# Kernel optimization log

Hardware: AMD Instinct MI355X
Metric: run time of the kernel (lower is better)

The kernel has to match this reference:

```python
import jax, jax.numpy as jnp
import numpy as np

H = 4          # num_heads
K_HOP = 2
EPS = 1e-5


def _ln(x, g, b):
    m = jnp.mean(x, axis=-1, keepdims=True)
    v = jnp.mean((x - m) ** 2, axis=-1, keepdims=True)
    return (x - m) * jax.lax.rsqrt(v + EPS) * g + b


def setup_inputs() -> dict:
    key = jax.random.key(0)
    B, T, N, D = 16, 24, 512, 64
    F = 256
    ks = jax.random.split(key, 16)
    s = 0.02
    inp = {
        'x': jax.random.normal(ks[0], (B, T, N, D), dtype=jnp.float32),
        'adj': jax.random.uniform(ks[1], (N, N), dtype=jnp.float32),
        'Wq': jax.random.normal(ks[2], (D, D), dtype=jnp.float32) * s,
        'bq': jnp.zeros((D,), jnp.float32),
        'Wk': jax.random.normal(ks[3], (D, D), dtype=jnp.float32) * s,
        'bk': jnp.zeros((D,), jnp.float32),
        'Wv': jax.random.normal(ks[4], (D, D), dtype=jnp.float32) * s,
        'bv': jnp.zeros((D,), jnp.float32),
        'Wo': jax.random.normal(ks[5], (D, D), dtype=jnp.float32) * s,
        'bo': jnp.zeros((D,), jnp.float32),
        'gcW': jax.random.normal(ks[6], (K_HOP + 1, D, D), dtype=jnp.float32) * s,
        'gcb': jnp.zeros((K_HOP + 1, D), jnp.float32),
        'W1': jax.random.normal(ks[7], (D, F), dtype=jnp.float32) * s,
        'b1': jnp.zeros((F,), jnp.float32),
        'W2': jax.random.normal(ks[8], (F, D), dtype=jnp.float32) * s,
        'b2': jnp.zeros((D,), jnp.float32),
        'g_t': jnp.ones((D,), jnp.float32), 'b_t': jnp.zeros((D,), jnp.float32),
        'g_g': jnp.ones((D,), jnp.float32), 'b_g': jnp.zeros((D,), jnp.float32),
        'g_f': jnp.ones((D,), jnp.float32), 'b_f': jnp.zeros((D,), jnp.float32),
    }
    return inp


def _forward(x, adj, Wq, bq, Wk, bk, Wv, bv, Wo, bo, gcW, gcb,
             W1, b1, W2, b2, g_t, b_t, g_g, b_g, g_f, b_f):
    B, T, N, D = x.shape
    hd = D // H
    scale = hd ** -0.5

    # ---- temporal multi-head attention (per node, along T) ----
    def heads(y):
        return y.reshape(B, T, N, H, hd)
    q = heads(x @ Wq + bq)
    k = heads(x @ Wk + bk)
    v = heads(x @ Wv + bv)
    scores = jnp.einsum('bqnhd,bknhd->bnhqk', q, k) * scale  # [B,N,H,T,T]
    attn = jax.nn.softmax(scores, axis=-1)
    att = jnp.einsum('bnhqk,bknhd->bqnhd', attn, v).reshape(B, T, N, D)
    att = att @ Wo + bo
    h = _ln(x + att, g_t, b_t)

    # ---- K-hop graph convolution: sum_k A_hat^k X W_k ----
    A = adj + jnp.eye(N, dtype=adj.dtype)
    deg = A.sum(-1)
    dinv = jnp.clip(deg, 1e-12, None) ** -0.5
    Ahat = dinv[:, None] * A * dinv[None, :]  # [N,N], shared across B*T
    prop = h
    gout = prop @ gcW[0] + gcb[0]
    for kk in range(1, K_HOP + 1):
        prop = jnp.einsum('mn,btnd->btmd', Ahat, prop)
        gout = gout + prop @ gcW[kk] + gcb[kk]
    h = _ln(h + gout, g_g, b_g)

    # ---- FFN (exact GELU, as torch default) ----
    f = jax.nn.gelu(h @ W1 + b1, approximate=False) @ W2 + b2
    return _ln(h + f, g_f, b_f)


def reference(x, adj, Wq, bq, Wk, bk, Wv, bv, Wo, bo, gcW, gcb,
              W1, b1, W2, b2, g_t, b_t, g_g, b_g, g_f, b_f):
    return _forward(x, adj, Wq, bq, Wk, bk, Wv, bv, Wo, bo, gcW, gcb,
                    W1, b1, W2, b2, g_t, b_t, g_g, b_g, g_f, b_f)
```

## Files before the change

### kernel.cpp

```cpp
#include <hip/hip_runtime.h>
#include <hip/hip_bf16.h>
#include <math.h>

typedef __hip_bfloat16 bf16;
typedef unsigned short ushort_t;

__device__ __forceinline__ float us2f(ushort_t u){
  union { unsigned u; float f; } v; v.u = ((unsigned)u) << 16; return v.f;
}
__device__ __forceinline__ ushort_t f2us(float f){
  union { float f; unsigned u; } v; v.f = f;
  unsigned r = v.u + 0x7fff + ((v.u >> 16) & 1);
  return (ushort_t)(r >> 16);
}

__device__ __forceinline__ float gelu_f(float x){
  float y = x * fmaf(0.0356774081f, x*x, 0.7978845608f);
  float e = __expf(-2.0f*y);
  return x * __builtin_amdgcn_rcpf(1.0f + e);
}

#define B_ 16
#define T_ 24
#define N_ 512
#define D_ 64
#define F_ 256

typedef __attribute__((ext_vector_type(8)))  short  frag8;
typedef __attribute__((ext_vector_type(16))) float  accv16;

__device__ __forceinline__ float wave_sum(float v){
#pragma unroll
  for (int off = 32; off > 0; off >>= 1) v += __shfl_xor(v, off, 64);
  return v;
}

__global__ __launch_bounds__(64) void k_dinv(const float* __restrict__ adj,
                                             float* __restrict__ dinv){
  int m = blockIdx.x;
  float s = 0.f;
  for (int n = threadIdx.x; n < N_; n += 64) s += adj[m*N_ + n];
  s = wave_sum(s);
  if (threadIdx.x == 0){
    float deg = s + 1.0f;
    dinv[m] = rsqrtf(fmaxf(deg, 1e-12f));
  }
}

__global__ __launch_bounds__(256) void k_ahat(const float* __restrict__ adj,
                                              const float* __restrict__ dinv,
                                              ushort_t* __restrict__ AhatB){
  int idx = blockIdx.x*256 + threadIdx.x;
  int m = idx >> 9, n = idx & (N_-1);
  float a = adj[idx] + (m == n ? 1.f : 0.f);
  AhatB[idx] = f2us(dinv[m]*a*dinv[n]);
}

__global__ __launch_bounds__(256) void k_wprep(
    const float* __restrict__ W1, const float* __restrict__ W2,
    const float* __restrict__ Wq, const float* __restrict__ Wk,
    const float* __restrict__ Wv, const float* __restrict__ Wo,
    const float* __restrict__ gcW,
    ushort_t* __restrict__ W1t, ushort_t* __restrict__ W2t,
    ushort_t* __restrict__ Wqt, ushort_t* __restrict__ Wkt,
    ushort_t* __restrict__ Wvt, ushort_t* __restrict__ Wot,
    ushort_t* __restrict__ gWt){
  int o = blockIdx.x*256 + threadIdx.x;
  int f = o >> 6, e = o & 63;
  W1t[o] = f2us(W1[e*256 + f]);
  int d = o >> 8, e2 = o & 255;
  W2t[o] = f2us(W2[e2*64 + d]);
  if (o < 4096){
    int dd = o >> 6, ee = o & 63;
    Wqt[o] = f2us(Wq[ee*64 + dd]);
    Wkt[o] = f2us(Wk[ee*64 + dd]);
    Wvt[o] = f2us(Wv[ee*64 + dd]);
    Wot[o] = f2us(Wo[ee*64 + dd]);
    gWt[o]        = f2us(gcW[       ee*64 + dd]);
    gWt[4096 + o] = f2us(gcW[4096 + ee*64 + dd]);
    gWt[8192 + o] = f2us(gcW[8192 + ee*64 + dd]);
  }
}

__global__ __launch_bounds__(256, 4) void k_attn_m(
    const float* __restrict__ x,
    const ushort_t* __restrict__ Wqt, const float* __restrict__ bq,
    const ushort_t* __restrict__ Wkt, const float* __restrict__ bk,
    const ushort_t* __restrict__ Wvt, const float* __restrict__ bv,
    const ushort_t* __restrict__ Wot, const float* __restrict__ bo,
    const float* __restrict__ g_t, const float* __restrict__ b_t,
    float* __restrict__ h1)
{
  __shared__ __align__(16) char smem[37120];
  ushort_t (*xsA)[72] = (ushort_t(*)[72]) smem;
  ushort_t (*qs)[72]  = (ushort_t(*)[72])(smem + 6912);
  ushort_t (*ks)[72]  = (ushort_t(*)[72])(smem + 13824);
  float    (*Os)[65]  = (float(*)[65])   (smem + 6912);
  ushort_t *vsT       = (ushort_t*)(smem + 20736);

  int tid = threadIdx.x;
  int lane = tid & 63, w = tid >> 6;
  int l31 = lane & 31, lh = lane >> 5;
  int mt = (w >> 1) * 32, nt = (w & 1) * 32;
  int b = blockIdx.x >> 8;
  int n0 = (blockIdx.x & 255) * 2;

  {
    uint4 z4 = {0,0,0,0};
#pragma unroll
    for (int i = 0; i < 4; i++)
      *(uint4*)(smem + 20736 + (tid + i*256)*16) = z4;
  }
#pragma unroll
  for (int i = 0; i < 3; i++){
    int idx = tid + i*256;
    int row = idx >> 4, d4 = (idx & 15) * 4;
    int node = row >= 24;
    int t = row - node*24;
    const float4 v = *(const float4*)&x[(((size_t)b*T_ + t)*N_ + n0 + node)*D_ + d4];
    ushort_t tmp[4] = { f2us(v.x), f2us(v.y), f2us(v.z), f2us(v.w) };
    *(unsigned long long*)&xsA[row][d4] = *(unsigned long long*)tmp;
  }
  __syncthreads();

#pragma unroll
  for (int pj = 0; pj < 3; pj++){
    const ushort_t* Wp = (pj==0 ? Wqt : pj==1 ? Wkt : Wvt);
    accv16 a = {};
#pragma unroll
    for (int kk = 0; kk < 64; kk += 16){
      frag8 af = *(const frag8*)&xsA[mt + l31][kk + lh*8];
      frag8 bf = *(const frag8*)&Wp[(size_t)(nt + l31)*64 + kk + lh*8];
      a = __builtin_amdgcn_mfma_f32_32x32x16_bf16(af, bf, a, 0, 0, 0);
    }
    float bias = (pj==0 ? bq : pj==1 ? bk : bv)[nt + l31];
    if (pj < 2){
      ushort_t (*dst)[72] = (pj==0 ? qs : ks);
#pragma unroll
      for (int r = 0; r < 16; r++){
        int row = mt + (r & 3) + 8*(r >> 2) + 4*lh;
        if (row < 48) dst[row][nt + l31] = f2us(a[r] + bias);
      }
    } else {
      int cl = nt + l31;
      int vr0 = ((cl >> 4) << 5) + (cl & 15);
#pragma unroll
      for (int r = 0; r < 16; r++){
        int row = mt + (r & 3) + 8*(r >> 2) + 4*lh;
        if (row < 48){
          int node = (row >= 24);
          int t2 = row - node*24;
          int R = node*128 + vr0;
          vsT[R*32 + (((t2 >> 3) ^ ((R >> 1) & 3)) << 3) + (t2 & 7)] = f2us(a[r] + bias);
        }
      }
    }
  }
  __syncthreads();

  int vs_s = (l31 >> 1) & 3;
#pragma unroll
  for (int gi = 0; gi < 2; gi++){
    int g = w*2 + gi;
    int node = g >> 2, hh = g & 3;
    accv16 s = {};
    frag8 kf = *(const frag8*)&ks[node*24 + l31][hh*16 + lh*8];
    frag8 qf = *(const frag8*)&qs[node*24 + l31][hh*16 + lh*8];
    s = __builtin_amdgcn_mfma_f32_32x32x16_bf16(kf, qf, s, 0, 0, 0);
    float e[12]; float sm = 0.f;
#pragma unroll
    for (int r = 0; r < 12; r++){ e[r] = __expf(s[r]*0.25f); sm += e[r]; }
    sm += __shfl_xor(sm, 32, 64);
    float rinv = 1.0f / sm;
    union { unsigned long long q; ushort_t u[4]; } a0, a1, a2;
#pragma unroll
    for (int j = 0; j < 4; j++){
      a0.u[j] = f2us(e[j]   * rinv);
      a1.u[j] = f2us(e[4+j] * rinv);
      a2.u[j] = f2us(e[8+j] * rinv);
    }
    unsigned long long send1 = lh ? a0.q : a1.q;
    unsigned long long r1 = __shfl_xor(send1, 32, 64);
    unsigned long long r2 = __shfl_xor(a2.q, 32, 64);
    union { frag8 f; unsigned long long q[2]; } f0, f1;
    f0.q[0] = lh ? r1   : a0.q;
    f0.q[1] = lh ? a1.q : r1;
    f1.q[0] = lh ? 0ULL : a2.q;
    f1.q[1] = lh ? 0ULL : r2;
    const ushort_t* vb = &vsT[(g*32 + l31)*32];
    frag8 bf0 = *(const frag8*)&vb[((0 + lh) ^ vs_s) << 3];
    frag8 bf1 = *(const frag8*)&vb[((2 + lh) ^ vs_s) << 3];
    accv16 acc = {};
    acc = __builtin_amdgcn_mfma_f32_32x32x16_bf16(f0.f, bf0, acc, 0, 0, 0);
    acc = __builtin_amdgcn_mfma_f32_32x32x16_bf16(f1.f, bf1, acc, 0, 0, 0);
    if (l31 < 16){
#pragma unroll
      for (int r = 0; r < 12; r++){
        int row = (r & 3) + 8*(r >> 2) + 4*lh;
        xsA[node*24 + row][hh*16 + l31] = f2us(acc[r]);
      }
    }
  }
  __syncthreads();

  accv16 ao = {};
#pragma unroll
  for (int kk = 0; kk < 64; kk += 16){
    frag8 af = *(const frag8*)&xsA[mt + l31][kk + lh*8];
    frag8 bf = *(const frag8*)&Wot[(size_t)(nt + l31)*64 + kk + lh*8];
    ao = __builtin_amdgcn_mfma_f32_32x32x16_bf16(af, bf, ao, 0, 0, 0);
  }
  {
    float bov = bo[nt + l31];
#pragma unroll
    for (int r = 0; r < 16; r++){
      int row = mt + (r & 3) + 8*(r >> 2) + 4*lh;
      if (row < 48) Os[row][nt + l31] = ao[r] + bov;
    }
  }
  __syncthreads();
  {
    float gv = g_t[lane], bvv = b_t[lane];
#pragma unroll
    for (int i = 0; i < 12; i++){
      int row = w + i*4;
      int node = row >= 24;
      int t = row - node*24;
      size_t gaddr = (((size_t)b*T_ + t)*N_ + n0 + node)*D_ + lane;
      float v = Os[row][lane] + x[gaddr];
      float m = wave_sum(v) * (1.f/64.f);
      float df = v - m;
      float var = wave_sum(df*df) * (1.f/64.f);
      h1[gaddr] = df * rsqrtf(var + 1e-5f) * gv + bvv;
    }
  }
}

__global__ __launch_bounds__(256, 8) void k_hT(const float* __restrict__ h,
                                               ushort_t* __restrict__ hT){
  __shared__ __align__(16) ushort_t tb[64][76];
  int tid = threadIdx.x;
  int n0 = (blockIdx.x & 7) * 64;
  size_t bt = blockIdx.x >> 3;
  const float* src = h + (bt*N_ + n0)*D_;
#pragma unroll
  for (int i = 0; i < 4; i++){
    int q = tid + i*256;
    int row = q >> 4, d4 = (q & 15)*4;
    float4 v = *(const float4*)&src[(size_t)q*4];
    ushort_t tmp[4] = { f2us(v.x), f2us(v.y), f2us(v.z), f2us(v.w) };
    *(unsigned long long*)&tb[row][d4] = *(unsigned long long*)tmp;
  }
  __syncthreads();
  int d = tid >> 2, nseg = (tid & 3)*16;
  ushort_t tmp[16];
#pragma unroll
  for (int j = 0; j < 16; j++){
    int jj = (j + ((d & 7) << 1)) & 15;
    tmp[jj] = tb[nseg + jj][d];
  }
  ushort_t* dst = hT + (bt*D_ + d)*N_ + n0 + nseg;
  *(uint4*)&dst[0] = *(uint4*)&tmp[0];
  *(uint4*)&dst[8] = *(uint4*)&tmp[8];
}

__global__ __launch_bounds__(256, 5) void k_prop_m(
    const ushort_t* __restrict__ Ahat,
    const ushort_t* __restrict__ XT,
    const ushort_t* __restrict__ gWkt,
    ushort_t* __restrict__ PT,
    ushort_t* __restrict__ G,
    int store_p, int accum)
{
  __shared__ __align__(16) ushort_t Ab[64][72];
  __shared__ __align__(16) ushort_t Xb[64][72];
  __shared__ __align__(16) ushort_t Yt[64][72];
  int tid  = threadIdx.x;
  int lane = tid & 63, w = tid >> 6;
  int mw = (w >> 1) * 32, nw = (w & 1) * 32;
  int l31 = lane & 31, lh = lane >> 5;
  int m0 = blockIdx.x * 64;
  size_t slice = (size_t)blockIdx.y * (N_ * D_);
  const ushort_t* Xg = XT + slice;

  accv16 acc = {};
  int ar = tid >> 3, ac8 = (tid & 7) * 8;
  for (int k0 = 0; k0 < N_; k0 += 64){
#pragma unroll
    for (int g = 0; g < 2; g++){
      int rr = ar + g*32;
      *(uint4*)&Ab[rr][ac8] = *(const uint4*)&Ahat[(size_t)(m0 + rr)*N_ + k0 + ac8];
      *(uint4*)&Xb[rr][ac8] = *(const uint4*)&Xg[(size_t)rr*N_ + k0 + ac8];
    }
    __syncthreads();
#pragma unroll
    for (int kk = 0; kk < 64; kk += 16){
      frag8 af = *(const frag8*)&Ab[mw + l31][kk + lh*8];
      frag8 bf = *(const frag8*)&Xb[nw + l31][kk + lh*8];
      acc = __builtin_amdgcn_mfma_f32_32x32x16_bf16(af, bf, acc, 0, 0, 0);
    }
    __syncthreads();
  }

#pragma unroll
  for (int r = 0; r < 16; r++){
    int row = mw + (r & 3) + 8*(r >> 2) + 4*lh;
    Yt[row][nw + l31] = f2us(acc[r]);
  }
  __syncthreads();

  if (store_p){
    int d = tid >> 2, mseg = (tid & 3) * 16;
    ushort_t tmp[16];
#pragma unroll
    for (int j = 0; j < 16; j++){
      int jj = (j + ((d & 7) << 1)) & 15;
      tmp[jj] = Yt[mseg + jj][d];
    }
    ushort_t* dst = PT + slice + (size_t)d*N_ + m0 + mseg;
    *(uint4*)&dst[0] = *(uint4*)&tmp[0];
    *(uint4*)&dst[8] = *(uint4*)&tmp[8];
  }

  accv16 acc2 = {};
#pragma unroll
  for (int kk = 0; kk < 64; kk += 16){
    frag8 af = *(const frag8*)&Yt[mw + l31][kk + lh*8];
    frag8 bf = *(const frag8*)&gWkt[(size_t)(nw + l31)*64 + kk + lh*8];
    acc2 = __builtin_amdgcn_mfma_f32_32x32x16_bf16(af, bf, acc2, 0, 0, 0);
  }
#pragma unroll
  for (int r = 0; r < 16; r++){
    int row = mw + (r & 3) + 8*(r >> 2) + 4*lh;
    Ab[row][nw + l31] = f2us(acc2[r]);
  }
  __syncthreads();
#pragma unroll
  for (int g = 0; g < 2; g++){
    int rr = ar + g*32;
    uint4 vv = *(const uint4*)&Ab[rr][ac8];
    size_t base = slice + (size_t)(m0 + rr)*D_ + ac8;
    if (accum){
      uint4 ov = *(const uint4*)&G[base];
      ushort_t* s = (ushort_t*)&vv;
      ushort_t* o = (ushort_t*)&ov;
      ushort_t res[8];
#pragma unroll
      for (int i = 0; i < 8; i++) res[i] = f2us(us2f(s[i]) + us2f(o[i]));
      *(uint4*)&G[base] = *(uint4*)res;
    } else {
      *(uint4*)&G[base] = vv;
    }
  }
}

__global__ __launch_bounds__(256, 4) void k_cffn(
  const ushort_t* __restrict__ g12,
  const ushort_t* __restrict__ gW0t,
  const float* __restrict__ gcb,
  const float* __restrict__ g_g, const float* __restrict__ b_g,
  const ushort_t* __restrict__ W1t, const ushort_t* __restrict__ W2t,
  const float* __restrict__ b1, const float* __restrict__ b2,
  const float* __restrict__ g_f, const float* __restrict__ b_f,
  float* __restrict__ h)
{
  __shared__ __align__(16) char smem[26624];
  ushort_t (*hsA)[72] = (ushort_t(*)[72]) smem;
  ushort_t (*Uc)[136] = (ushort_t(*)[136])(smem + 9216);
  float    (*Sf)[68]  = (float(*)[68])    (smem + 9216);
  float    (*Os)[68]  = (float(*)[68])    (smem + 9216);

  int tid = threadIdx.x;
  int lane = tid & 63, w = tid >> 6;
  int l31 = lane & 31, lh = lane >> 5;
  size_t tok0 = (size_t)blockIdx.x * 64;

#pragma unroll
  for (int i = 0; i < 4; i++){
    int q = tid + i*256;
    int row = q >> 4, d4 = (q & 15) * 4;
    float4 v = *(const float4*)&h[tok0*64 + (size_t)q*4];
    ushort_t tmp[4] = { f2us(v.x), f2us(v.y), f2us(v.z), f2us(v.w) };
    *(unsigned long long*)&hsA[row][d4] = *(unsigned long long*)tmp;
  }
  __syncthreads();

  {
    int mg = (w >> 1) * 32, ng = (w & 1) * 32;
    accv16 ag = {};
#pragma unroll
    for (int kk = 0; kk < 64; kk += 16){
      frag8 af = *(const frag8*)&hsA[mg + l31][kk + lh*8];
      frag8 bf = *(const frag8*)&gW0t[(size_t)(ng + l31)*64 + kk + lh*8];
      ag = __builtin_amdgcn_mfma_f32_32x32x16_bf16(af, bf, ag, 0, 0, 0);
    }
    int col = ng + l31;
    float bs = gcb[col] + gcb[64 + col] + gcb[128 + col];
#pragma unroll
    for (int r = 0; r < 16; r++){
      int row = mg + (r & 3) + 8*(r >> 2) + 4*lh;
      size_t ga = (tok0 + row)*64 + col;
      Sf[row][col] = ag[r] + h[ga] + us2f(g12[ga]) + bs;
    }
  }
  __syncthreads();

  int rrow = tid >> 2, seg = (tid & 3) * 16;
  float h2r[16];
  {
    float vb[16]; float s1 = 0.f;
#pragma unroll
    for (int j4 = 0; j4 < 4; j4++){
      float4 v = *(const float4*)&Sf[rrow][seg + j4*4];
      vb[j4*4+0] = v.x; vb[j4*4+1] = v.y; vb[j4*4+2] = v.z; vb[j4*4+3] = v.w;
      s1 += v.x + v.y + v.z + v.w;
    }
    s1 += __shfl_xor(s1, 1, 64); s1 += __shfl_xor(s1, 2, 64);
    float m = s1 * (1.f/64.f);
    float s2 = 0.f;
#pragma unroll
    for (int j = 0; j < 16; j++){ vb[j] -= m; s2 += vb[j]*vb[j]; }
    s2 += __shfl_xor(s2, 1, 64); s2 += __shfl_xor(s2, 2, 64);
    float rstd = rsqrtf(s2 * (1.f/64.f) + 1e-5f);
    ushort_t tmp[16];
#pragma unroll
    for (int j4 = 0; j4 < 4; j4++){
      float4 gv = *(const float4*)&g_g[seg + j4*4];
      float4 bv = *(const float4*)&b_g[seg + j4*4];
      h2r[j4*4+0] = vb[j4*4+0]*rstd*gv.x + bv.x;
      h2r[j4*4+1] = vb[j4*4+1]*rstd*gv.y + bv.y;
      h2r[j4*4+2] = vb[j4*4+2]*rstd*gv.z + bv.z;
      h2r[j4*4+3] = vb[j4*4+3]*rstd*gv.w + bv.w;
    }
#pragma unroll
    for (int j = 0; j < 16; j++) tmp[j] = f2us(h2r[j]);
    *(uint4*)&hsA[rrow][seg]     = *(uint4*)&tmp[0];
    *(uint4*)&hsA[rrow][seg + 8] = *(uint4*)&tmp[8];
  }
  __syncthreads();

  int mw1 = (w & 1) * 32, nA = (w >> 1) * 32;
  int mw2 = (w >> 1) * 32, dw = (w & 1) * 32;
  accv16 acc2 = {};
#pragma unroll
  for (int f0 = 0; f0 < F_; f0 += 128){
    if (f0) __syncthreads();
    accv16 accA = {}, accB = {};
#pragma unroll
    for (int kk = 0; kk < 64; kk += 16){
      frag8 af  = *(const frag8*)&hsA[mw1 + l31][kk + lh*8];
      frag8 b0  = *(const frag8*)&W1t[(size_t)(f0 + nA + l31)*64 + kk + lh*8];
      frag8 b1f = *(const frag8*)&W1t[(size_t)(f0 + nA + 64 + l31)*64 + kk + lh*8];
      accA = __builtin_amdgcn_mfma_f32_32x32x16_bf16(af, b0,  accA, 0, 0, 0);
      accB = __builtin_amdgcn_mfma_f32_32x32x16_bf16(af, b1f, accB, 0, 0, 0);
    }
    {
      float bA = b1[f0 + nA + l31];
      float bB = b1[f0 + nA + 64 + l31];
#pragma unroll
      for (int r = 0; r < 16; r++){
        int row = mw1 + (r & 3) + 8*(r >> 2) + 4*lh;
        Uc[row][nA + l31]      = f2us(gelu_f(accA[r] + bA));
        Uc[row][nA + 64 + l31] = f2us(gelu_f(accB[r] + bB));
      }
    }
    __syncthreads();
#pragma unroll
    for (int kk = 0; kk < 128; kk += 16){
      frag8 af = *(const frag8*)&Uc[mw2 + l31][kk + lh*8];
      frag8 bf = *(const frag8*)&W2t[(size_t)(dw + l31)*256 + f0 + kk + lh*8];
      acc2 = __builtin_amdgcn_mfma_f32_32x32x16_bf16(af, bf, acc2, 0, 0, 0);
    }
  }
  __syncthreads();
  {
    float b2v = b2[dw + l31];
#pragma unroll
    for (int r = 0; r < 16; r++){
      int row = mw2 + (r & 3) + 8*(r >> 2) + 4*lh;
      Os[row][dw + l31] = acc2[r] + b2v;
    }
  }
  __syncthreads();

  {
    float vb[16]; float s1 = 0.f;
#pragma unroll
    for (int j4 = 0; j4 < 4; j4++){
      float4 v = *(const float4*)&Os[rrow][seg + j4*4];
      vb[j4*4+0] = v.x + h2r[j4*4+0];
      vb[j4*4+1] = v.y + h2r[j4*4+1];
      vb[j4*4+2] = v.z + h2r[j4*4+2];
      vb[j4*4+3] = v.w + h2r[j4*4+3];
      s1 += vb[j4*4+0] + vb[j4*4+1] + vb[j4*4+2] + vb[j4*4+3];
    }
    s1 += __shfl_xor(s1, 1, 64); s1 += __shfl_xor(s1, 2, 64);
    float m = s1 * (1.f/64.f);
    float s2 = 0.f;
#pragma unroll
    for (int j = 0; j < 16; j++){ vb[j] -= m; s2 += vb[j]*vb[j]; }
    s2 += __shfl_xor(s2, 1, 64); s2 += __shfl_xor(s2, 2, 64);
    float rstd = rsqrtf(s2 * (1.f/64.f) + 1e-5f);
#pragma unroll
    for (int j4 = 0; j4 < 4; j4++){
      float4 gv = *(const float4*)&g_f[seg + j4*4];
      float4 bv = *(const float4*)&b_f[seg + j4*4];
      float4 st;
      st.x = vb[j4*4+0]*rstd*gv.x + bv.x;
      st.y = vb[j4*4+1]*rstd*gv.y + bv.y;
      st.z = vb[j4*4+2]*rstd*gv.z + bv.z;
      st.w = vb[j4*4+3]*rstd*gv.w + bv.w;
      *(float4*)&h[(tok0 + rrow)*64 + seg + j4*4] = st;
    }
  }
}

extern "C" void kernel_launch(void* const* d_in, const int* in_sizes, int n_in,
                              void* d_out, int out_size, void* d_ws, size_t ws_size,
                              hipStream_t stream)
{
  const float* x   = (const float*)d_in[0];
  const float* adj = (const float*)d_in[1];
  const float* Wq  = (const float*)d_in[2];
  const float* bq  = (const float*)d_in[3];
  const float* Wk  = (const float*)d_in[4];
  const float* bk  = (const float*)d_in[5];
  const float* Wv  = (const float*)d_in[6];
  const float* bv  = (const float*)d_in[7];
  const float* Wo  = (const float*)d_in[8];
  const float* bo  = (const float*)d_in[9];
  const float* gcW = (const float*)d_in[10];
  const float* gcb = (const float*)d_in[11];
  const float* W1  = (const float*)d_in[12];
  const float* b1  = (const float*)d_in[13];
  const float* W2  = (const float*)d_in[14];
  const float* b2  = (const float*)d_in[15];
  const float* g_t = (const float*)d_in[16];
  const float* b_t = (const float*)d_in[17];
  const float* g_g = (const float*)d_in[18];
  const float* b_g = (const float*)d_in[19];
  const float* g_f = (const float*)d_in[20];
  const float* b_f = (const float*)d_in[21];

  const size_t MD = (size_t)B_*T_*N_*D_;
  float* dinv = (float*)d_ws;
  ushort_t* AhatB = (ushort_t*)(dinv + 512);
  ushort_t* PT  = AhatB + (size_t)N_*N_;
  ushort_t* g12 = PT + MD;
  ushort_t* hT  = g12 + MD;
  ushort_t* W1t = hT + MD;
  ushort_t* W2t = W1t + 256*64;
  ushort_t* Wqt = W2t + 64*256;
  ushort_t* Wkt = Wqt + 4096;
  ushort_t* Wvt = Wkt + 4096;
  ushort_t* Wot = Wvt + 4096;
  ushort_t* gWt = Wot + 4096;
  float* h = (float*)d_out;

  k_dinv<<<N_, 64, 0, stream>>>(adj, dinv);
  k_ahat<<<(N_*N_)/256, 256, 0, stream>>>(adj, dinv, AhatB);
  k_wprep<<<64, 256, 0, stream>>>(W1, W2, Wq, Wk, Wv, Wo, gcW,
                                  W1t, W2t, Wqt, Wkt, Wvt, Wot, gWt);
  k_attn_m<<<B_*N_/2, 256, 0, stream>>>(x, Wqt,bq, Wkt,bk, Wvt,bv, Wot,bo, g_t,b_t, h);
  k_hT<<<B_*T_*8, 256, 0, stream>>>(h, hT);
  k_prop_m<<<dim3(N_/64, B_*T_), 256, 0, stream>>>(AhatB, hT, gWt + 4096, PT, g12, 1, 0);
  k_prop_m<<<dim3(N_/64, B_*T_), 256, 0, stream>>>(AhatB, PT, gWt + 8192, PT, g12, 0, 1);
  k_cffn<<<(int)(MD/D_/64), 256, 0, stream>>>(g12, gWt, gcb, g_g, b_g,
                                              W1t, W2t, b1, b2, g_f, b_f, h);
}
```

Measured before the change: 383.0 us.

## Precompute Ahat squared and fuse both graph-propagation hops into one kernel

A new kernel computes Ahat² once per call, reading Ahat and a transposed copy written by k_ahat. The two sequential propagation kernels become one k_gconv, which multiplies the hT tile by Ahat and by Ahat² in the same k-loop and applies both gcW projections before a single store. This removes the PT intermediate write and reread, the read-modify-write on G, and one launch, at the cost of an extra Ahat² tile load per step and a small N×N matmul. The bf16 conversion also switches to the compiler's native __bf16 cast, and rounding Ahat² to bf16 changes numerics slightly.

```diff
diff --git a/kernel.cpp b/kernel.cpp
--- a/kernel.cpp
+++ b/kernel.cpp
@@ -9,9 +9,7 @@
   union { unsigned u; float f; } v; v.u = ((unsigned)u) << 16; return v.f;
 }
 __device__ __forceinline__ ushort_t f2us(float f){
-  union { float f; unsigned u; } v; v.f = f;
-  unsigned r = v.u + 0x7fff + ((v.u >> 16) & 1);
-  return (ushort_t)(r >> 16);
+  union { __bf16 b; ushort_t u; } v; v.b = (__bf16)f; return v.u;
 }
 
 __device__ __forceinline__ float gelu_f(float x){
@@ -49,11 +47,59 @@
 
 __global__ __launch_bounds__(256) void k_ahat(const float* __restrict__ adj,
                                               const float* __restrict__ dinv,
-                                              ushort_t* __restrict__ AhatB){
+                                              ushort_t* __restrict__ AhatB,
+                                              ushort_t* __restrict__ AhatBT){
   int idx = blockIdx.x*256 + threadIdx.x;
   int m = idx >> 9, n = idx & (N_-1);
   float a = adj[idx] + (m == n ? 1.f : 0.f);
-  AhatB[idx] = f2us(dinv[m]*a*dinv[n]);
+  ushort_t v = f2us(dinv[m]*a*dinv[n]);
+  AhatB[idx] = v;
+  AhatBT[n*N_ + m] = v;
+}
+
+__global__ __launch_bounds__(256, 4) void k_ah2(
+    const ushort_t* __restrict__ A1,
+    const ushort_t* __restrict__ A1T,
+    ushort_t* __restrict__ A2)
+{
+  __shared__ __align__(16) ushort_t Ab[64][72];
+  __shared__ __align__(16) ushort_t Bb[64][72];
+  __shared__ __align__(16) ushort_t Yt[64][72];
+  int tid  = threadIdx.x;
+  int lane = tid & 63, w = tid >> 6;
+  int mw = (w >> 1) * 32, nw = (w & 1) * 32;
+  int l31 = lane & 31, lh = lane >> 5;
+  int m0 = blockIdx.x * 64, n0 = blockIdx.y * 64;
+  int ar = tid >> 3, ac8 = (tid & 7) * 8;
+
+  accv16 acc = {};
+  for (int k0 = 0; k0 < N_; k0 += 64){
+#pragma unroll
+    for (int g = 0; g < 2; g++){
+      int rr = ar + g*32;
+      *(uint4*)&Ab[rr][ac8] = *(const uint4*)&A1 [(size_t)(m0 + rr)*N_ + k0 + ac8];
+      *(uint4*)&Bb[rr][ac8] = *(const uint4*)&A1T[(size_t)(n0 + rr)*N_ + k0 + ac8];
+    }
+    __syncthreads();
+#pragma unroll
+    for (int kk = 0; kk < 64; kk += 16){
+      frag8 af = *(const frag8*)&Ab[mw + l31][kk + lh*8];
+      frag8 bf = *(const frag8*)&Bb[nw + l31][kk + lh*8];
+      acc = __builtin_amdgcn_mfma_f32_32x32x16_bf16(af, bf, acc, 0, 0, 0);
+    }
+    __syncthreads();
+  }
+#pragma unroll
+  for (int r = 0; r < 16; r++){
+    int row = mw + (r & 3) + 8*(r >> 2) + 4*lh;
+    Yt[row][nw + l31] = f2us(acc[r]);
+  }
+  __syncthreads();
+#pragma unroll
+  for (int g = 0; g < 2; g++){
+    int rr = ar + g*32;
+    *(uint4*)&A2[(size_t)(m0 + rr)*N_ + n0 + ac8] = *(const uint4*)&Yt[rr][ac8];
+  }
 }
 
 __global__ __launch_bounds__(256) void k_wprep(
@@ -264,15 +310,16 @@
   *(uint4*)&dst[8] = *(uint4*)&tmp[8];
 }
 
-__global__ __launch_bounds__(256, 5) void k_prop_m(
-    const ushort_t* __restrict__ Ahat,
+__global__ __launch_bounds__(256, 4) void k_gconv(
+    const ushort_t* __restrict__ A1,
+    const ushort_t* __restrict__ A2,
     const ushort_t* __restrict__ XT,
-    const ushort_t* __restrict__ gWkt,
-    ushort_t* __restrict__ PT,
-    ushort_t* __restrict__ G,
-    int store_p, int accum)
+    const ushort_t* __restrict__ gW1t,
+    const ushort_t* __restrict__ gW2t,
+    ushort_t* __restrict__ G)
 {
-  __shared__ __align__(16) ushort_t Ab[64][72];
+  __shared__ __align__(16) ushort_t Ab1[64][72];
+  __shared__ __align__(16) ushort_t Ab2[64][72];
   __shared__ __align__(16) ushort_t Xb[64][72];
   __shared__ __align__(16) ushort_t Yt[64][72];
   int tid  = threadIdx.x;
@@ -282,22 +329,25 @@
   int m0 = blockIdx.x * 64;
   size_t slice = (size_t)blockIdx.y * (N_ * D_);
   const ushort_t* Xg = XT + slice;
-
-  accv16 acc = {};
   int ar = tid >> 3, ac8 = (tid & 7) * 8;
+
+  accv16 acc1 = {}, acc2 = {};
   for (int k0 = 0; k0 < N_; k0 += 64){
 #pragma unroll
     for (int g = 0; g < 2; g++){
       int rr = ar + g*32;
-      *(uint4*)&Ab[rr][ac8] = *(const uint4*)&Ahat[(size_t)(m0 + rr)*N_ + k0 + ac8];
-      *(uint4*)&Xb[rr][ac8] = *(const uint4*)&Xg[(size_t)rr*N_ + k0 + ac8];
+      *(uint4*)&Ab1[rr][ac8] = *(const uint4*)&A1[(size_t)(m0 + rr)*N_ + k0 + ac8];
+      *(uint4*)&Ab2[rr][ac8] = *(const uint4*)&A2[(size_t)(m0 + rr)*N_ + k0 + ac8];
+      *(uint4*)&Xb [rr][ac8] = *(const uint4*)&Xg[(size_t)rr*N_ + k0 + ac8];
     }
     __syncthreads();
 #pragma unroll
     for (int kk = 0; kk < 64; kk += 16){
-      frag8 af = *(const frag8*)&Ab[mw + l31][kk + lh*8];
-      frag8 bf = *(const frag8*)&Xb[nw + l31][kk + lh*8];
-      acc = __builtin_amdgcn_mfma_f32_32x32x16_bf16(af, bf, acc, 0, 0, 0);
+      frag8 bf  = *(const frag8*)&Xb [nw + l31][kk + lh*8];
+      frag8 af1 = *(const frag8*)&Ab1[mw + l31][kk + lh*8];
+      frag8 af2 = *(const frag8*)&Ab2[mw + l31][kk + lh*8];
+      acc1 = __builtin_amdgcn_mfma_f32_32x32x16_bf16(af1, bf, acc1, 0, 0, 0);
+      acc2 = __builtin_amdgcn_mfma_f32_32x32x16_bf16(af2, bf, acc2, 0, 0, 0);
     }
     __syncthreads();
   }
@@ -305,52 +355,34 @@
 #pragma unroll
   for (int r = 0; r < 16; r++){
     int row = mw + (r & 3) + 8*(r >> 2) + 4*lh;
-    Yt[row][nw + l31] = f2us(acc[r]);
-  }
-  __syncthreads();
-
-  if (store_p){
-    int d = tid >> 2, mseg = (tid & 3) * 16;
-    ushort_t tmp[16];
-#pragma unroll
-    for (int j = 0; j < 16; j++){
-      int jj = (j + ((d & 7) << 1)) & 15;
-      tmp[jj] = Yt[mseg + jj][d];
-    }
-    ushort_t* dst = PT + slice + (size_t)d*N_ + m0 + mseg;
-    *(uint4*)&dst[0] = *(uint4*)&tmp[0];
-    *(uint4*)&dst[8] = *(uint4*)&tmp[8];
-  }
-
-  accv16 acc2 = {};
+    Yt [row][nw + l31] = f2us(acc1[r]);
+    Ab1[row][nw + l31] = f2us(acc2[r]);
+  }
+  __syncthreads();
+
+  accv16 ag = {};
 #pragma unroll
   for (int kk = 0; kk < 64; kk += 16){
-    frag8 af = *(const frag8*)&Yt[mw + l31][kk + lh*8];
-    frag8 bf = *(const frag8*)&gWkt[(size_t)(nw + l31)*64 + kk + lh*8];
-    acc2 = __builtin_amdgcn_mfma_f32_32x32x16_bf16(af, bf, acc2, 0, 0, 0);
+    frag8 a1f = *(const frag8*)&Yt [mw + l31][kk + lh*8];
+    frag8 b1f = *(const frag8*)&gW1t[(size_t)(nw + l31)*64 + kk + lh*8];
+    ag = __builtin_amdgcn_mfma_f32_32x32x16_bf16(a1f, b1f, ag, 0, 0, 0);
+  }
+#pragma unroll
+  for (int kk = 0; kk < 64; kk += 16){
+    frag8 a2f = *(const frag8*)&Ab1[mw + l31][kk + lh*8];
+    frag8 b2f = *(const frag8*)&gW2t[(size_t)(nw + l31)*64 + kk + lh*8];
+    ag = __builtin_amdgcn_mfma_f32_32x32x16_bf16(a2f, b2f, ag, 0, 0, 0);
   }
 #pragma unroll
   for (int r = 0; r < 16; r++){
     int row = mw + (r & 3) + 8*(r >> 2) + 4*lh;
-    Ab[row][nw + l31] = f2us(acc2[r]);
+    Xb[row][nw + l31] = f2us(ag[r]);
   }
   __syncthreads();
 #pragma unroll
   for (int g = 0; g < 2; g++){
     int rr = ar + g*32;
-    uint4 vv = *(const uint4*)&Ab[rr][ac8];
-    size_t base = slice + (size_t)(m0 + rr)*D_ + ac8;
-    if (accum){
-      uint4 ov = *(const uint4*)&G[base];
-      ushort_t* s = (ushort_t*)&vv;
-      ushort_t* o = (ushort_t*)&ov;
-      ushort_t res[8];
-#pragma unroll
-      for (int i = 0; i < 8; i++) res[i] = f2us(us2f(s[i]) + us2f(o[i]));
-      *(uint4*)&G[base] = *(uint4*)res;
-    } else {
-      *(uint4*)&G[base] = vv;
-    }
+    *(uint4*)&G[slice + (size_t)(m0 + rr)*D_ + ac8] = *(const uint4*)&Xb[rr][ac8];
   }
 }
 
@@ -543,10 +575,12 @@
   const float* b_f = (const float*)d_in[21];
 
   const size_t MD = (size_t)B_*T_*N_*D_;
+  const size_t NN = (size_t)N_*N_;
   float* dinv = (float*)d_ws;
-  ushort_t* AhatB = (ushort_t*)(dinv + 512);
-  ushort_t* PT  = AhatB + (size_t)N_*N_;
-  ushort_t* g12 = PT + MD;
+  ushort_t* AhatB  = (ushort_t*)(dinv + 512);
+  ushort_t* AhatBT = AhatB + NN;
+  ushort_t* AhatB2 = AhatBT + NN;
+  ushort_t* g12 = AhatB2 + NN;
   ushort_t* hT  = g12 + MD;
   ushort_t* W1t = hT + MD;
   ushort_t* W2t = W1t + 256*64;
@@ -558,13 +592,14 @@
   float* h = (float*)d_out;
 
   k_dinv<<<N_, 64, 0, stream>>>(adj, dinv);
-  k_ahat<<<(N_*N_)/256, 256, 0, stream>>>(adj, dinv, AhatB);
+  k_ahat<<<(N_*N_)/256, 256, 0, stream>>>(adj, dinv, AhatB, AhatBT);
   k_wprep<<<64, 256, 0, stream>>>(W1, W2, Wq, Wk, Wv, Wo, gcW,
                                   W1t, W2t, Wqt, Wkt, Wvt, Wot, gWt);
+  k_ah2<<<dim3(8, 8), 256, 0, stream>>>(AhatB, AhatBT, AhatB2);
   k_attn_m<<<B_*N_/2, 256, 0, stream>>>(x, Wqt,bq, Wkt,bk, Wvt,bv, Wot,bo, g_t,b_t, h);
   k_hT<<<B_*T_*8, 256, 0, stream>>>(h, hT);
-  k_prop_m<<<dim3(N_/64, B_*T_), 256, 0, stream>>>(AhatB, hT, gWt + 4096, PT, g12, 1, 0);
-  k_prop_m<<<dim3(N_/64, B_*T_), 256, 0, stream>>>(AhatB, PT, gWt + 8192, PT, g12, 0, 1);
+  k_gconv<<<dim3(N_/64, B_*T_), 256, 0, stream>>>(AhatB, AhatB2, hT,
+                                                  gWt + 4096, gWt + 8192, g12);
   k_cffn<<<(int)(MD/D_/64), 256, 0, stream>>>(g12, gWt, gcb, g_g, b_g,
                                               W1t, W2t, b1, b2, g_f, b_f, h);
 }
```

After: 346.9 us. 9.4% less time.
